# Kernel tuning notes

Hardware: AMD Instinct MI355X
Metric: run time of the kernel (lower is better)

Reference implementation:

```python
import jax, jax.numpy as jnp
import numpy as np

IN_CH, HID_CH, OUT_CH, NUM_REL = 128, 256, 128, 8
N_NODES, N_EDGES = 50000, 800000


def _glorot(key, shape):
    fan_in, fan_out = shape[-2], shape[-1]
    lim = float(np.sqrt(6.0 / (fan_in + fan_out)))
    return jax.random.uniform(key, shape, jnp.float32, -lim, lim)


def setup_inputs() -> dict:
    key = jax.random.key(0)
    ks = jax.random.split(key, 12)
    x = jax.random.normal(ks[0], (N_NODES, IN_CH), jnp.float32)
    edge_index = jax.random.randint(ks[1], (2, N_EDGES), 0, N_NODES, jnp.int32)
    edge_type = jax.random.randint(ks[2], (N_EDGES,), 0, NUM_REL, jnp.int32)
    return {
        "x": x, "edge_index": edge_index, "edge_type": edge_type,
        "W1": _glorot(ks[3], (NUM_REL, IN_CH, HID_CH)),
        "root1": _glorot(ks[4], (IN_CH, HID_CH)),
        "b1": jnp.zeros((HID_CH,), jnp.float32),
        "W2": _glorot(ks[5], (NUM_REL, HID_CH, HID_CH)),
        "root2": _glorot(ks[6], (HID_CH, HID_CH)),
        "b2": jnp.zeros((HID_CH,), jnp.float32),
        "W3": _glorot(ks[7], (NUM_REL, HID_CH, OUT_CH)),
        "root3": _glorot(ks[8], (HID_CH, OUT_CH)),
        "b3": jnp.zeros((OUT_CH,), jnp.float32),
    }


def _rgcn_conv(x, src, dst, etype, W, root, b):
    # PyG RGCNConv: per-relation mean aggregation of neighbor features,
    # per-relation linear transform, plus root weight and bias.
    # Linear commutes with mean, so aggregate raw x[src] per (dst, relation)
    # then contract with W: sum_r mean_agg[:, r] @ W[r].
    n, d = x.shape
    r = W.shape[0]
    seg = dst.astype(jnp.int32) * r + etype.astype(jnp.int32)  # [E]
    msg = x[src]                                               # [E, d] gather
    agg = jax.ops.segment_sum(msg, seg, num_segments=n * r)    # [N*R, d]
    cnt = jax.ops.segment_sum(jnp.ones((msg.shape[0],), x.dtype), seg,
                              num_segments=n * r)              # [N*R]
    mean = agg / jnp.maximum(cnt, 1.0)[:, None]                # [N*R, d]
    mean = mean.reshape(n, r, d)
    out = jnp.einsum('nrd,rdo->no', mean, W) + x @ root + b
    return out


def reference(x, edge_index, edge_type, W1, root1, b1, W2, root2, b2, W3, root3, b3):
    src, dst = edge_index[0], edge_index[1]
    h = jax.nn.relu(_rgcn_conv(x, src, dst, edge_type, W1, root1, b1))
    # dropout is identity in eval mode
    h = jax.nn.relu(_rgcn_conv(h, src, dst, edge_type, W2, root2, b2))
    out = _rgcn_conv(h, src, dst, edge_type, W3, root3, b3)
    return out
```

## Files before the change

kernel.cpp:

```cpp
#include <hip/hip_runtime.h>

#define NREL 8
#define SCHUNK 2048

typedef __attribute__((ext_vector_type(8))) short bf16x8;
typedef __attribute__((ext_vector_type(4))) float f32x4;

__device__ __forceinline__ float bf2f(ushort u) {
  union { unsigned u; float f; } c; c.u = ((unsigned)u) << 16; return c.f;
}
__device__ __forceinline__ ushort f2bf(float f) {
  union { float f; unsigned u; } c; c.f = f;
  unsigned r = c.u + 0x7FFFu + ((c.u >> 16) & 1u);
  return (ushort)(r >> 16);
}

__global__ void hist_k(const int* __restrict__ dst, const int* __restrict__ et,
                       int* __restrict__ cnt, int nE) {
  int i = blockIdx.x * blockDim.x + threadIdx.x;
  if (i < nE) atomicAdd(&cnt[dst[i] * NREL + et[i]], 1);
}

__global__ void scan1_k(const int* __restrict__ cnt, int n,
                        int* __restrict__ thexc, int* __restrict__ bsum) {
  __shared__ int sh[256];
  int b = blockIdx.x, t = threadIdx.x;
  int base = b * SCHUNK + t * 8;
  int s = 0;
#pragma unroll
  for (int j = 0; j < 8; ++j) { int idx = base + j; s += (idx < n) ? cnt[idx] : 0; }
  sh[t] = s;
  __syncthreads();
  for (int d = 1; d < 256; d <<= 1) {
    int v = (t >= d) ? sh[t - d] : 0;
    __syncthreads();
    sh[t] += v;
    __syncthreads();
  }
  thexc[b * 256 + t] = sh[t] - s;
  if (t == 255) bsum[b] = sh[255];
}

__global__ void scan2_k(int* __restrict__ bsum, int nb, int total,
                        int* __restrict__ off, int n) {
  int run = 0;
  for (int i = 0; i < nb; ++i) { int v = bsum[i]; bsum[i] = run; run += v; }
  off[n] = total;
}

__global__ void scan3_k(const int* __restrict__ cnt, int n, const int* __restrict__ thexc,
                        const int* __restrict__ bsum, int* __restrict__ off,
                        int* __restrict__ cur) {
  int b = blockIdx.x, t = threadIdx.x;
  int base = b * SCHUNK + t * 8;
  int run = bsum[b] + thexc[b * 256 + t];
#pragma unroll
  for (int j = 0; j < 8; ++j) {
    int idx = base + j;
    if (idx < n) { int c = cnt[idx]; off[idx] = run; cur[idx] = run; run += c; }
  }
}

__global__ void fill2_k(const int* __restrict__ src, const int* __restrict__ dst,
                        const int* __restrict__ et, int nE,
                        int* __restrict__ cur, int* __restrict__ slist) {
  int i = blockIdx.x * blockDim.x + threadIdx.x;
  if (i < nE) {
    int seg = dst[i] * NREL + et[i];
    int p = atomicAdd(&cur[seg], 1);
    slist[p] = src[i];
  }
}

__global__ void f2b_k(const float* __restrict__ in, ushort* __restrict__ out, int n4) {
  int i = blockIdx.x * blockDim.x + threadIdx.x;
  if (i < n4) {
    float4 v = *(const float4*)(in + (size_t)i * 4);
    ushort4 o;
    o.x = f2bf(v.x); o.y = f2bf(v.y); o.z = f2bf(v.z); o.w = f2bf(v.w);
    *(ushort4*)(out + (size_t)i * 4) = o;
  }
}

__global__ void wt_k(const float* __restrict__ W, ushort* __restrict__ Wt,
                     int R, int K, int O, int G) {
  size_t i = (size_t)blockIdx.x * blockDim.x + threadIdx.x;
  size_t tot = (size_t)R * K * O;
  if (i >= tot) return;
  int o = (int)(i % O);
  size_t t = i / O;
  int d = (int)(t % K);
  int r = (int)(t / K);
  Wt[((size_t)(r / G) * O + o) * ((size_t)G * K) + (size_t)(r % G) * K + d] = f2bf(W[i]);
}

template<int D, int NR>
__global__ void gatherN_k(const ushort* __restrict__ xb, const int* __restrict__ slist,
                          const int* __restrict__ off, int r0,
                          ushort* __restrict__ agg, int N) {
  constexpr int V = D / 64;
  const int lane = threadIdx.x & 63;
  const int d = (blockIdx.x * blockDim.x + threadIdx.x) >> 6;
  if (d >= N) return;
  int o[NR + 1];
#pragma unroll
  for (int j = 0; j <= NR; ++j) o[j] = off[d * NREL + r0 + j];
  const int bc = lane * V;
  float s[NR][V];
#pragma unroll
  for (int r = 0; r < NR; ++r)
#pragma unroll
    for (int v = 0; v < V; ++v) s[r][v] = 0.f;

  const int base = o[0], total = o[NR] - base;
  for (int i0 = 0; i0 < total; i0 += 4) {
    uint  raw2[4];
    uint2 raw4[4];
#pragma unroll
    for (int u = 0; u < 4; ++u) {
      if (i0 + u < total) {
        int e = slist[base + i0 + u];
        const ushort* xp = xb + (size_t)e * D + bc;
        if constexpr (V == 2) raw2[u] = *(const uint*)xp;
        else                  raw4[u] = *(const uint2*)xp;
      }
    }
#pragma unroll
    for (int u = 0; u < 4; ++u) {
      if (i0 + u < total) {
        int gj = base + i0 + u;
        float f[V];
        if constexpr (V == 2) {
          f[0] = bf2f((ushort)(raw2[u] & 0xffff));
          f[1] = bf2f((ushort)(raw2[u] >> 16));
        } else {
          f[0] = bf2f((ushort)(raw4[u].x & 0xffff));
          f[1] = bf2f((ushort)(raw4[u].x >> 16));
          f[2] = bf2f((ushort)(raw4[u].y & 0xffff));
          f[3] = bf2f((ushort)(raw4[u].y >> 16));
        }
#pragma unroll
        for (int r = 0; r < NR; ++r) {
          if (gj >= o[r] && gj < o[r + 1]) {
#pragma unroll
            for (int v = 0; v < V; ++v) s[r][v] += f[v];
          }
        }
      }
    }
  }

#pragma unroll
  for (int r = 0; r < NR; ++r) {
    int c = o[r + 1] - o[r];
    float w = 1.f / (float)(c > 1 ? c : 1);
    ushort* mp = agg + (size_t)d * (NR * D) + r * D + bc;
    if constexpr (V == 2) {
      ushort2 st; st.x = f2bf(s[r][0] * w); st.y = f2bf(s[r][1] * w);
      *(ushort2*)mp = st;
    } else {
      ushort4 st; st.x = f2bf(s[r][0] * w); st.y = f2bf(s[r][1] * w);
      st.z = f2bf(s[r][2] * w); st.w = f2bf(s[r][3] * w);
      *(ushort4*)mp = st;
    }
  }
}

template<bool CF32>
__global__ __launch_bounds__(256)
void mgemm_k(const ushort* __restrict__ A, int K, const ushort* __restrict__ Bt,
             const float* __restrict__ bias, void* __restrict__ Cv,
             int loadC, int relu, int M, int O) {
  __shared__ ushort Al[128 * 64];
  __shared__ ushort Bl[128 * 64];
  const int tid = threadIdx.x;
  const int lane = tid & 63;
  const int w = tid >> 6;
  const int wr = (w >> 1) * 64;
  const int wc = (w & 1) * 64;
  const int m0 = blockIdx.x * 128;
  const int n0 = blockIdx.y * 128;

  f32x4 acc[4][4];
#pragma unroll
  for (int i = 0; i < 4; ++i)
#pragma unroll
    for (int j = 0; j < 4; ++j) acc[i][j] = (f32x4){0.f, 0.f, 0.f, 0.f};

  const int srow = tid >> 3;
  const int schk = tid & 7;

  uint4 ra[4], rb[4];
  auto gload = [&](int k0) {
#pragma unroll
    for (int p = 0; p < 4; ++p) {
      int row = p * 32 + srow;
      int gm = m0 + row;
      ra[p] = make_uint4(0, 0, 0, 0);
      if (gm < M) ra[p] = *(const uint4*)(A + (size_t)gm * K + k0 + schk * 8);
      rb[p] = *(const uint4*)(Bt + (size_t)(n0 + row) * K + k0 + schk * 8);
    }
  };
  auto swrite = [&]() {
#pragma unroll
    for (int p = 0; p < 4; ++p) {
      int row = p * 32 + srow;
      *(uint4*)&Al[row * 64 + ((schk ^ (row & 7)) * 8)] = ra[p];
      *(uint4*)&Bl[row * 64 + ((schk ^ (row & 7)) * 8)] = rb[p];
    }
  };

  gload(0);
  const int nt = K >> 6;
  for (int t = 0; t < nt; ++t) {
    swrite();
    __syncthreads();
    if (t + 1 < nt) gload((t + 1) << 6);
#pragma unroll
    for (int kk = 0; kk < 2; ++kk) {
      bf16x8 a_f[4], b_f[4];
      int slot = kk * 4 + (lane >> 4);
#pragma unroll
      for (int f = 0; f < 4; ++f) {
        int mr = wr + f * 16 + (lane & 15);
        a_f[f] = *(const bf16x8*)&Al[mr * 64 + ((slot ^ (mr & 7)) * 8)];
        int nc = wc + f * 16 + (lane & 15);
        b_f[f] = *(const bf16x8*)&Bl[nc * 64 + ((slot ^ (nc & 7)) * 8)];
      }
#pragma unroll
      for (int i = 0; i < 4; ++i)
#pragma unroll
        for (int j = 0; j < 4; ++j)
          acc[i][j] = __builtin_amdgcn_mfma_f32_16x16x32_bf16(a_f[i], b_f[j], acc[i][j], 0, 0, 0);
    }
    __syncthreads();
  }

  float bv[4];
#pragma unroll
  for (int j = 0; j < 4; ++j) bv[j] = bias ? bias[n0 + wc + j * 16 + (lane & 15)] : 0.f;
#pragma unroll
  for (int i = 0; i < 4; ++i) {
#pragma unroll
    for (int rg = 0; rg < 4; ++rg) {
      int row = m0 + wr + i * 16 + (lane >> 4) * 4 + rg;
      if (row < M) {
#pragma unroll
        for (int j = 0; j < 4; ++j) {
          int col = n0 + wc + j * 16 + (lane & 15);
          float v = acc[i][j][rg] + bv[j];
          if (CF32) {
            float* C = (float*)Cv + (size_t)row * O + col;
            if (loadC) v += *C;
            if (relu) v = fmaxf(v, 0.f);
            *C = v;
          } else {
            ushort* C = (ushort*)Cv + (size_t)row * O + col;
            if (loadC) v += bf2f(*C);
            if (relu) v = fmaxf(v, 0.f);
            *C = f2bf(v);
          }
        }
      }
    }
  }
}

extern "C" void kernel_launch(void* const* d_in, const int* in_sizes, int n_in,
                              void* d_out, int out_size, void* d_ws, size_t ws_size,
                              hipStream_t stream) {
  const float* x  = (const float*)d_in[0];
  const int* eidx = (const int*)d_in[1];
  const int* etyp = (const int*)d_in[2];
  const float* W1 = (const float*)d_in[3];
  const float* r1 = (const float*)d_in[4];
  const float* b1 = (const float*)d_in[5];
  const float* W2 = (const float*)d_in[6];
  const float* r2 = (const float*)d_in[7];
  const float* b2 = (const float*)d_in[8];
  const float* W3 = (const float*)d_in[9];
  const float* r3 = (const float*)d_in[10];
  const float* b3 = (const float*)d_in[11];
  float* out = (float*)d_out;

  const int N = in_sizes[0] / 128;
  const int E = in_sizes[2];
  const int* src = eidx;
  const int* dst = eidx + E;
  const int NSEG = N * NREL;
  const int NB = (NSEG + SCHUNK - 1) / SCHUNK;
  (void)n_in; (void)out_size;

  auto al = [](size_t v) { return (v + 255) & ~(size_t)255; };
  char* p = (char*)d_ws;
  int* cnt    = (int*)p;    p += al((size_t)NSEG * 4);
  int* off    = (int*)p;    p += al((size_t)(NSEG + 1) * 4);
  int* thexc  = (int*)p;    p += al((size_t)NB * 256 * 4);
  int* bsum   = (int*)p;    p += al((size_t)NB * 4);
  int* slist  = (int*)p;    p += al((size_t)E * 4);
  ushort* xb  = (ushort*)p; p += al((size_t)N * 128 * 2);
  ushort* h1  = (ushort*)p; p += al((size_t)N * 256 * 2);
  ushort* h2  = (ushort*)p; p += al((size_t)N * 256 * 2);
  ushort* agg = (ushort*)p; p += al((size_t)N * 1024 * 2);
  ushort* wt1 = (ushort*)p; p += al((size_t)NREL * 128 * 256 * 2);
  ushort* rt1 = (ushort*)p; p += al((size_t)128 * 256 * 2);
  ushort* wt2 = (ushort*)p; p += al((size_t)NREL * 256 * 256 * 2);
  ushort* rt2 = (ushort*)p; p += al((size_t)256 * 256 * 2);
  ushort* wt3 = (ushort*)p; p += al((size_t)NREL * 256 * 128 * 2);
  ushort* rt3 = (ushort*)p; p += al((size_t)256 * 128 * 2);
  size_t used = (size_t)(p - (char*)d_ws);
  if (used > ws_size) return;

  hipMemsetAsync(d_ws, 0, used, stream);

  hist_k<<<(E + 255) / 256, 256, 0, stream>>>(dst, etyp, cnt, E);
  scan1_k<<<NB, 256, 0, stream>>>(cnt, NSEG, thexc, bsum);
  scan2_k<<<1, 1, 0, stream>>>(bsum, NB, E, off, NSEG);
  scan3_k<<<NB, 256, 0, stream>>>(cnt, NSEG, thexc, bsum, off, cnt);
  fill2_k<<<(E + 255) / 256, 256, 0, stream>>>(src, dst, etyp, E, cnt, slist);

  f2b_k<<<(N * 128 / 4 + 255) / 256, 256, 0, stream>>>(x, xb, N * 128 / 4);
  auto wconv = [&](const float* W, ushort* Wt, int R, int K, int O, int G) {
    size_t tot = (size_t)R * K * O;
    wt_k<<<(int)((tot + 255) / 256), 256, 0, stream>>>(W, Wt, R, K, O, G);
  };
  wconv(W1, wt1, NREL, 128, 256, 8);
  wconv(r1, rt1, 1, 128, 256, 1);
  wconv(W2, wt2, NREL, 256, 256, 4);
  wconv(r2, rt2, 1, 256, 256, 1);
  wconv(W3, wt3, NREL, 256, 128, 4);
  wconv(r3, rt3, 1, 256, 128, 1);

  const int gblocks = (N * 64 + 255) / 256;

  auto layer = [&](const ushort* xin, int D, int NP, const ushort* Wt, const ushort* Rt,
                   const float* bias, void* Y, int O, bool relu, bool cf32) {
    dim3 g((N + 127) / 128, O / 128);
    if (cf32)
      mgemm_k<true><<<g, 256, 0, stream>>>(xin, D, Rt, bias, Y, 0, 0, N, O);
    else
      mgemm_k<false><<<g, 256, 0, stream>>>(xin, D, Rt, bias, Y, 0, 0, N, O);
    int NR = NREL / NP;
    for (int pass = 0; pass < NP; ++pass) {
      if (D == 128)
        gatherN_k<128, 8><<<gblocks, 256, 0, stream>>>(xin, slist, off, pass * 8, agg, N);
      else
        gatherN_k<256, 4><<<gblocks, 256, 0, stream>>>(xin, slist, off, pass * 4, agg, N);
      const ushort* Bt = Wt + (size_t)pass * O * (NR * D);
      int rl = (relu && pass == NP - 1) ? 1 : 0;
      if (cf32)
        mgemm_k<true><<<g, 256, 0, stream>>>(agg, NR * D, Bt, nullptr, Y, 1, rl, N, O);
      else
        mgemm_k<false><<<g, 256, 0, stream>>>(agg, NR * D, Bt, nullptr, Y, 1, rl, N, O);
    }
  };

  layer(xb, 128, 1, wt1, rt1, b1, h1, 256, true,  false);
  layer(h1, 256, 2, wt2, rt2, b2, h2, 256, true,  false);
  layer(h2, 256, 2, wt3, rt3, b3, out, 128, false, true);
}
```

Before: 1.186 ms.

## Fuse root GEMM into first aggregation GEMM and double-buffer global prefetch

The separate root-weight GEMM launch (x @ root + bias) is removed. It is folded into the first relation pass by concatenating a second A/B operand pair along K inside mgemm_k, so the output is no longer stored and then reloaded through loadC. The register prefetch also becomes two stages deep, loading tile t+2 while tile t is computed. This saves one kernel launch and one full output read-modify-write per layer, at the cost of more registers for the doubled prefetch buffers, which may lower occupancy.

```diff
diff --git a/kernel.cpp b/kernel.cpp
--- a/kernel.cpp
+++ b/kernel.cpp
@@ -168,7 +168,8 @@
 
 template<bool CF32>
 __global__ __launch_bounds__(256)
-void mgemm_k(const ushort* __restrict__ A, int K, const ushort* __restrict__ Bt,
+void mgemm_k(const ushort* __restrict__ A1, int K1, const ushort* __restrict__ B1t,
+             const ushort* __restrict__ A2, int K2, const ushort* __restrict__ B2t,
              const float* __restrict__ bias, void* __restrict__ Cv,
              int loadC, int relu, int M, int O) {
   __shared__ ushort Al[128 * 64];
@@ -190,32 +191,39 @@
   const int srow = tid >> 3;
   const int schk = tid & 7;
 
-  uint4 ra[4], rb[4];
-  auto gload = [&](int k0) {
+  const int nt1 = K1 >> 6;
+  const int nt2 = A2 ? (K2 >> 6) : 0;
+  const int nt = nt1 + nt2;
+
+  uint4 ra[2][4], rb[2][4];
+  auto gload = [&](int t, int s) {
+    const ushort* PA; const ushort* PB; int Kk, k0;
+    if (t < nt1) { PA = A1; PB = B1t; Kk = K1; k0 = t << 6; }
+    else         { PA = A2; PB = B2t; Kk = K2; k0 = (t - nt1) << 6; }
 #pragma unroll
     for (int p = 0; p < 4; ++p) {
       int row = p * 32 + srow;
       int gm = m0 + row;
-      ra[p] = make_uint4(0, 0, 0, 0);
-      if (gm < M) ra[p] = *(const uint4*)(A + (size_t)gm * K + k0 + schk * 8);
-      rb[p] = *(const uint4*)(Bt + (size_t)(n0 + row) * K + k0 + schk * 8);
+      ra[s][p] = make_uint4(0, 0, 0, 0);
+      if (gm < M) ra[s][p] = *(const uint4*)(PA + (size_t)gm * Kk + k0 + schk * 8);
+      rb[s][p] = *(const uint4*)(PB + (size_t)(n0 + row) * Kk + k0 + schk * 8);
     }
   };
-  auto swrite = [&]() {
+  auto swrite = [&](int s) {
 #pragma unroll
     for (int p = 0; p < 4; ++p) {
       int row = p * 32 + srow;
-      *(uint4*)&Al[row * 64 + ((schk ^ (row & 7)) * 8)] = ra[p];
-      *(uint4*)&Bl[row * 64 + ((schk ^ (row & 7)) * 8)] = rb[p];
+      *(uint4*)&Al[row * 64 + ((schk ^ (row & 7)) * 8)] = ra[s][p];
+      *(uint4*)&Bl[row * 64 + ((schk ^ (row & 7)) * 8)] = rb[s][p];
     }
   };
 
-  gload(0);
-  const int nt = K >> 6;
+  gload(0, 0);
+  if (nt > 1) gload(1, 1);
   for (int t = 0; t < nt; ++t) {
-    swrite();
+    swrite(t & 1);
     __syncthreads();
-    if (t + 1 < nt) gload((t + 1) << 6);
+    if (t + 2 < nt) gload(t + 2, t & 1);
 #pragma unroll
     for (int kk = 0; kk < 2; ++kk) {
       bf16x8 a_f[4], b_f[4];
@@ -336,10 +344,6 @@
   auto layer = [&](const ushort* xin, int D, int NP, const ushort* Wt, const ushort* Rt,
                    const float* bias, void* Y, int O, bool relu, bool cf32) {
     dim3 g((N + 127) / 128, O / 128);
-    if (cf32)
-      mgemm_k<true><<<g, 256, 0, stream>>>(xin, D, Rt, bias, Y, 0, 0, N, O);
-    else
-      mgemm_k<false><<<g, 256, 0, stream>>>(xin, D, Rt, bias, Y, 0, 0, N, O);
     int NR = NREL / NP;
     for (int pass = 0; pass < NP; ++pass) {
       if (D == 128)
@@ -347,11 +351,16 @@
       else
         gatherN_k<256, 4><<<gblocks, 256, 0, stream>>>(xin, slist, off, pass * 4, agg, N);
       const ushort* Bt = Wt + (size_t)pass * O * (NR * D);
+      const ushort* A2 = (pass == 0) ? xin : nullptr;
+      const ushort* B2 = (pass == 0) ? Rt : nullptr;
+      const float* bs  = (pass == 0) ? bias : nullptr;
       int rl = (relu && pass == NP - 1) ? 1 : 0;
       if (cf32)
-        mgemm_k<true><<<g, 256, 0, stream>>>(agg, NR * D, Bt, nullptr, Y, 1, rl, N, O);
+        mgemm_k<true><<<g, 256, 0, stream>>>(agg, NR * D, Bt, A2, D, B2, bs, Y,
+                                             pass > 0, rl, N, O);
       else
-        mgemm_k<false><<<g, 256, 0, stream>>>(agg, NR * D, Bt, nullptr, Y, 1, rl, N, O);
+        mgemm_k<false><<<g, 256, 0, stream>>>(agg, NR * D, Bt, A2, D, B2, bs, Y,
+                                              pass > 0, rl, N, O);
     }
   };
 
```

After: 1.649 ms. 39.1% more time.
